# Kernel tuning notes

Hardware: AMD Instinct MI355X
Metric: run time of the kernel (lower is better)

## Reference

```python
import jax, jax.numpy as jnp
import numpy as np

V, E, H, L, T, B = 6500, 192, 6, 6, 512, 32
HS = E // H  # 32
EPS = 1e-5


def setup_inputs() -> dict:
    key = jax.random.key(0)
    ks = jax.random.split(key, 9)
    s = 0.02
    return {
        "idx": jax.random.randint(ks[0], (B, T), 0, V, dtype=jnp.int32),
        "tok_emb": jax.random.normal(ks[1], (V, E), dtype=jnp.float32) * s,
        "Wq": jax.random.normal(ks[2], (L, E, E), dtype=jnp.float32) * s,
        "Wk": jax.random.normal(ks[3], (L, E, E), dtype=jnp.float32) * s,
        "Wv": jax.random.normal(ks[4], (L, E, E), dtype=jnp.float32) * s,
        "Wo": jax.random.normal(ks[5], (L, E, E), dtype=jnp.float32) * s,
        "W1": jax.random.normal(ks[6], (L, E, 4 * E), dtype=jnp.float32) * s,
        "W2": jax.random.normal(ks[7], (L, 4 * E, E), dtype=jnp.float32) * s,
        "ln1_g": jnp.ones((L, E)), "ln1_b": jnp.zeros((L, E)),
        "ln2_g": jnp.ones((L, E)), "ln2_b": jnp.zeros((L, E)),
        "lnf_g": jnp.ones((E,)), "lnf_b": jnp.zeros((E,)),
        "Wlm": jax.random.normal(ks[8], (E, V), dtype=jnp.float32) * s,
    }


def _layer_norm(x, g, b):
    mu = jnp.mean(x, axis=-1, keepdims=True)
    var = jnp.mean(jnp.square(x - mu), axis=-1, keepdims=True)
    return (x - mu) * jax.lax.rsqrt(var + EPS) * g + b


def _sinusoidal(t, d):
    pos = jnp.arange(t, dtype=jnp.float32)[:, None]
    div = jnp.exp(jnp.arange(0, d, 2, dtype=jnp.float32) * (-np.log(10000.0) / d))
    pe = jnp.zeros((t, d), dtype=jnp.float32)
    pe = pe.at[:, 0::2].set(jnp.sin(pos * div))
    pe = pe.at[:, 1::2].set(jnp.cos(pos * div))
    return pe


def reference(idx, tok_emb, Wq, Wk, Wv, Wo, W1, W2,
              ln1_g, ln1_b, ln2_g, ln2_b, lnf_g, lnf_b, Wlm):
    x = tok_emb[idx] + _sinusoidal(T, E)[None, :, :]  # [B,T,E]
    mask = jnp.tril(jnp.ones((T, T), dtype=bool))
    scale = E ** (-0.5)  # NOTE: original scales by n_embd**-0.5, not head_size

    def block(x, p):
        l1g, l1b, wq, wk, wv, wo, l2g, l2b, w1, w2 = p
        h = _layer_norm(x, l1g, l1b)
        q = jnp.einsum('bte,ehd->bhtd', h, wq.reshape(E, H, HS))
        k = jnp.einsum('bte,ehd->bhtd', h, wk.reshape(E, H, HS))
        v = jnp.einsum('bte,ehd->bhtd', h, wv.reshape(E, H, HS))
        wei = jnp.einsum('bhtd,bhsd->bhts', q, k) * scale  # [B,H,T,T]
        wei = jnp.where(mask, wei, -jnp.inf)
        wei = jax.nn.softmax(wei, axis=-1)
        att = jnp.einsum('bhts,bhsd->bthd', wei, v).reshape(B, T, E)
        x = x + att @ wo
        h2 = _layer_norm(x, l2g, l2b)
        x = x + jax.nn.gelu(h2 @ w1, approximate=False) @ w2
        return x, None

    x, _ = jax.lax.scan(block, x, (ln1_g, ln1_b, Wq, Wk, Wv, Wo, ln2_g, ln2_b, W1, W2))
    x = _layer_norm(x, lnf_g, lnf_b)
    return x @ Wlm  # [B,T,V] logits
```

## Files before the change

### kernel.cpp

```cpp
#include <hip/hip_runtime.h>
#include <hip/hip_bf16.h>
#include <math.h>

#define VOCAB 6500
#define EMB   192
#define NH    6
#define NL    6
#define SEQ   512
#define BATCH 32
#define HSZ   32
#define BT    (BATCH*SEQ)

typedef __attribute__((ext_vector_type(8))) short bh8;
typedef __attribute__((ext_vector_type(4))) float f32x4;

__global__ __launch_bounds__(256) void embed_ln(
    const int* __restrict__ idx, const float* __restrict__ tok,
    const float* __restrict__ g, const float* __restrict__ b,
    float* __restrict__ x, __hip_bfloat16* __restrict__ h) {
  const int wid = threadIdx.x >> 6, lane = threadIdx.x & 63;
  const int bt = blockIdx.x * 4 + wid;
  const int t  = bt & (SEQ - 1);
  const int tokid = idx[bt];
  float v[3];
  #pragma unroll
  for (int i = 0; i < 3; ++i) {
    const int e = lane + i * 64;
    const int i2 = e & ~1;
    const float div = expf((float)i2 * (-9.210340371976184f / (float)EMB));
    const float ang = (float)t * div;
    const float pe  = (e & 1) ? cosf(ang) : sinf(ang);
    v[i] = tok[(size_t)tokid * EMB + e] + pe;
  }
  float s = v[0] + v[1] + v[2];
  #pragma unroll
  for (int o = 32; o; o >>= 1) s += __shfl_xor(s, o);
  const float mu = s * (1.0f / (float)EMB);
  float vs = 0.f;
  #pragma unroll
  for (int i = 0; i < 3; ++i) { const float d = v[i] - mu; vs += d * d; }
  #pragma unroll
  for (int o = 32; o; o >>= 1) vs += __shfl_xor(vs, o);
  const float r = rsqrtf(vs * (1.0f / (float)EMB) + 1e-5f);
  float* xr = x + (size_t)bt * EMB;
  __hip_bfloat16* hr = h + (size_t)bt * EMB;
  #pragma unroll
  for (int i = 0; i < 3; ++i) {
    const int e = lane + i * 64;
    xr[e] = v[i];
    hr[e] = __float2bfloat16((v[i] - mu) * r * g[e] + b[e]);
  }
}

__global__ __launch_bounds__(256) void wcast(
    const float* __restrict__ W, __hip_bfloat16* __restrict__ Wt,
    int K, int N, int dstride) {
  __shared__ float t[32][33];
  const float* Ws = W + (size_t)blockIdx.z * K * N;
  __hip_bfloat16* Wd = Wt + (size_t)blockIdx.z * dstride * K;
  const int kt = blockIdx.y * 32, nt = blockIdx.x * 32;
  const int tx = threadIdx.x, ty = threadIdx.y;
  for (int i = ty; i < 32; i += 8) {
    const int k = kt + i, n = nt + tx;
    t[i][tx] = (k < K && n < N) ? Ws[(size_t)k * N + n] : 0.f;
  }
  __syncthreads();
  for (int i = ty; i < 32; i += 8) {
    const int n = nt + i, k = kt + tx;
    if (n < N && k < K) Wd[(size_t)n * K + k] = __float2bfloat16(t[tx][i]);
  }
}

__global__ __launch_bounds__(256) void wcast4(
    const float* __restrict__ Wq, const float* __restrict__ Wk,
    const float* __restrict__ Wv, const float* __restrict__ Wo,
    __hip_bfloat16* __restrict__ wqkv, __hip_bfloat16* __restrict__ wot) {
  __shared__ float t[32][33];
  const int z = blockIdx.z, sel = z / NL, layer = z % NL;
  const float* srcs[4] = {Wq, Wk, Wv, Wo};
  const float* Ws = srcs[sel] + (size_t)layer * EMB * EMB;
  __hip_bfloat16* Wd = (sel < 3)
      ? wqkv + ((size_t)layer * 576 + sel * 192) * EMB
      : wot  + (size_t)layer * EMB * EMB;
  const int kt = blockIdx.y * 32, nt = blockIdx.x * 32;
  const int tx = threadIdx.x, ty = threadIdx.y;
  for (int i = ty; i < 32; i += 8)
    t[i][tx] = Ws[(size_t)(kt + i) * EMB + nt + tx];
  __syncthreads();
  for (int i = ty; i < 32; i += 8)
    Wd[(size_t)(nt + i) * EMB + kt + tx] = __float2bfloat16(t[tx][i]);
}

template<int EPI, int BN>
__global__ __launch_bounds__(256) void gemm_big(
    const __hip_bfloat16* __restrict__ A, const __hip_bfloat16* __restrict__ Bt,
    void* __restrict__ Cv, int M, int N, int K) {
  constexpr int LDK = 72;
  constexpr int NB = BN / 32;
  constexpr int NC = BN / 16;
  __shared__ short As[128 * LDK];
  __shared__ short Bs[BN * LDK];
  const int tid = threadIdx.x;
  const int wid = tid >> 6, lane = tid & 63;
  const int m0 = blockIdx.y * 128, n0 = blockIdx.x * BN;
  const int srow = tid >> 3, schk = tid & 7;
  const int fr = lane & 15, fg = lane >> 4;

  f32x4 acc[2][NC];
  #pragma unroll
  for (int rt = 0; rt < 2; ++rt)
    #pragma unroll
    for (int ct = 0; ct < NC; ++ct) acc[rt][ct] = (f32x4){0.f, 0.f, 0.f, 0.f};

  for (int k0 = 0; k0 < K; k0 += 64) {
    bh8 av[4], bv[NB];
    #pragma unroll
    for (int p = 0; p < 4; ++p)
      av[p] = *reinterpret_cast<const bh8*>(A + (size_t)(m0 + srow + p * 32) * K + k0 + schk * 8);
    #pragma unroll
    for (int p = 0; p < NB; ++p) {
      const int nr = n0 + srow + p * 32;
      if (nr < N) bv[p] = *reinterpret_cast<const bh8*>(Bt + (size_t)nr * K + k0 + schk * 8);
      else        bv[p] = (bh8){0,0,0,0,0,0,0,0};
    }
    __syncthreads();
    #pragma unroll
    for (int p = 0; p < 4; ++p)
      *reinterpret_cast<bh8*>(As + (srow + p * 32) * LDK + schk * 8) = av[p];
    #pragma unroll
    for (int p = 0; p < NB; ++p)
      *reinterpret_cast<bh8*>(Bs + (srow + p * 32) * LDK + schk * 8) = bv[p];
    __syncthreads();
    #pragma unroll
    for (int s = 0; s < 2; ++s) {
      bh8 af[2];
      #pragma unroll
      for (int rt = 0; rt < 2; ++rt)
        af[rt] = *reinterpret_cast<const bh8*>(As + (wid * 32 + rt * 16 + fr) * LDK + s * 32 + fg * 8);
      #pragma unroll
      for (int ct = 0; ct < NC; ++ct) {
        const bh8 bf_ = *reinterpret_cast<const bh8*>(Bs + (ct * 16 + fr) * LDK + s * 32 + fg * 8);
        #pragma unroll
        for (int rt = 0; rt < 2; ++rt)
          acc[rt][ct] = __builtin_amdgcn_mfma_f32_16x16x32_bf16(af[rt], bf_, acc[rt][ct], 0, 0, 0);
      }
    }
  }

  #pragma unroll
  for (int rt = 0; rt < 2; ++rt)
    #pragma unroll
    for (int ct = 0; ct < NC; ++ct) {
      const int col = n0 + ct * 16 + fr;
      if (col < N) {
        #pragma unroll
        for (int rr = 0; rr < 4; ++rr) {
          const int row = m0 + wid * 32 + rt * 16 + fg * 4 + rr;
          float v = acc[rt][ct][rr];
          if (EPI == 0) {
            ((float*)Cv)[(size_t)row * N + col] = v;
          } else if (EPI == 2) {
            v = 0.5f * v * (1.0f + erff(v * 0.70710678118654752f));
            ((__hip_bfloat16*)Cv)[(size_t)row * N + col] = __float2bfloat16(v);
          } else {
            const int part = col / 192, c2 = col - part * 192;
            const int bb = row >> 9, tt = row & (SEQ - 1);
            const int hh = c2 >> 5, dd = c2 & (HSZ - 1);
            ((__hip_bfloat16*)Cv)[(size_t)part * BT * EMB +
                (((size_t)(bb * NH + hh)) * SEQ + tt) * HSZ + dd] = __float2bfloat16(v);
          }
        }
      }
    }
}

__global__ __launch_bounds__(256) void gemm_resln(
    const __hip_bfloat16* __restrict__ A, const __hip_bfloat16* __restrict__ Bt,
    float* __restrict__ X, __hip_bfloat16* __restrict__ Hout,
    const float* __restrict__ g, const float* __restrict__ b, int K) {
  constexpr int LDK = 72;
  __shared__ short As[64 * LDK];
  __shared__ short Bs[192 * LDK];
  const int tid = threadIdx.x;
  const int wid = tid >> 6, lane = tid & 63;
  const int m0 = blockIdx.x * 64;
  const int srow = tid >> 3, schk = tid & 7;
  const int fr = lane & 15, fg = lane >> 4;

  f32x4 acc[12];
  #pragma unroll
  for (int j = 0; j < 12; ++j) acc[j] = (f32x4){0.f, 0.f, 0.f, 0.f};

  for (int k0 = 0; k0 < K; k0 += 64) {
    bh8 av[2], bv[6];
    #pragma unroll
    for (int p = 0; p < 2; ++p)
      av[p] = *reinterpret_cast<const bh8*>(A + (size_t)(m0 + srow + p * 32) * K + k0 + schk * 8);
    #pragma unroll
    for (int p = 0; p < 6; ++p)
      bv[p] = *reinterpret_cast<const bh8*>(Bt + (size_t)(srow + p * 32) * K + k0 + schk * 8);
    __syncthreads();
    #pragma unroll
    for (int p = 0; p < 2; ++p)
      *reinterpret_cast<bh8*>(As + (srow + p * 32) * LDK + schk * 8) = av[p];
    #pragma unroll
    for (int p = 0; p < 6; ++p)
      *reinterpret_cast<bh8*>(Bs + (srow + p * 32) * LDK + schk * 8) = bv[p];
    __syncthreads();
    #pragma unroll
    for (int s = 0; s < 2; ++s) {
      const bh8 af = *reinterpret_cast<const bh8*>(As + (wid * 16 + fr) * LDK + s * 32 + fg * 8);
      #pragma unroll
      for (int j = 0; j < 12; ++j) {
        const bh8 bf_ = *reinterpret_cast<const bh8*>(Bs + (j * 16 + fr) * LDK + s * 32 + fg * 8);
        acc[j] = __builtin_amdgcn_mfma_f32_16x16x32_bf16(af, bf_, acc[j], 0, 0, 0);
      }
    }
  }

  #pragma unroll
  for (int rr = 0; rr < 4; ++rr) {
    const int row = m0 + wid * 16 + fg * 4 + rr;
    float v[12], sum = 0.f, sq = 0.f;
    #pragma unroll
    for (int j = 0; j < 12; ++j) {
      v[j] = acc[j][rr] + X[(size_t)row * EMB + j * 16 + fr];
      sum += v[j]; sq += v[j] * v[j];
    }
    #pragma unroll
    for (int o = 8; o; o >>= 1) {
      sum += __shfl_xor(sum, o);
      sq  += __shfl_xor(sq,  o);
    }
    const float mu = sum * (1.0f / (float)EMB);
    const float r  = rsqrtf(sq * (1.0f / (float)EMB) - mu * mu + 1e-5f);
    #pragma unroll
    for (int j = 0; j < 12; ++j) {
      const int col = j * 16 + fr;
      X[(size_t)row * EMB + col] = v[j];
      Hout[(size_t)row * EMB + col] = __float2bfloat16((v[j] - mu) * r * g[col] + b[col]);
    }
  }
}

__global__ __launch_bounds__(256) void flash_attn(
    const __hip_bfloat16* __restrict__ qh, const __hip_bfloat16* __restrict__ kh,
    const __hip_bfloat16* __restrict__ vh, __hip_bfloat16* __restrict__ att) {
  constexpr int QT = 128, KT = 64, LDP = 72;
  __shared__ __hip_bfloat16 Ks[KT * LDP];
  __shared__ __hip_bfloat16 Vs[HSZ * LDP];
  __shared__ __hip_bfloat16 Ps[4][32 * LDP];
  const int qt = blockIdx.x, h = blockIdx.y, b = blockIdx.z;
  const int tid = threadIdx.x, wid = tid >> 6, lane = tid & 63;
  const int q0 = qt * QT;
  const size_t hb = ((size_t)(b * NH + h)) * SEQ * HSZ;
  const int fr = lane & 15, fg = lane >> 4;
  const float SCALE = 0.07216878364870323f;

  bh8 aq[2];
  #pragma unroll
  for (int rt = 0; rt < 2; ++rt)
    aq[rt] = *reinterpret_cast<const bh8*>(
        qh + hb + (size_t)(q0 + wid * 32 + rt * 16 + fr) * HSZ + fg * 8);

  f32x4 o[2][2];
  float m[2][4], l[2][4];
  #pragma unroll
  for (int rt = 0; rt < 2; ++rt) {
    #pragma unroll
    for (int ct = 0; ct < 2; ++ct) o[rt][ct] = (f32x4){0.f, 0.f, 0.f, 0.f};
    #pragma unroll
    for (int rr = 0; rr < 4; ++rr) { m[rt][rr] = -1e30f; l[rt][rr] = 0.f; }
  }

  const int nt = 2 * qt + 2;
  const int sr = tid >> 2, d0 = (tid & 3) * 8;
  for (int it = 0; it < nt; ++it) {
    const int s0 = it * KT;
    __syncthreads();
    {
      const bh8 kv8 = *reinterpret_cast<const bh8*>(kh + hb + (size_t)(s0 + sr) * HSZ + d0);
      *reinterpret_cast<bh8*>(&Ks[sr * LDP + d0]) = kv8;
      const bh8 vv8 = *reinterpret_cast<const bh8*>(vh + hb + (size_t)(s0 + sr) * HSZ + d0);
      short tmp[8]; *reinterpret_cast<bh8*>(tmp) = vv8;
      #pragma unroll
      for (int j = 0; j < 8; ++j)
        Vs[(d0 + j) * LDP + sr] = *reinterpret_cast<__hip_bfloat16*>(&tmp[j]);
    }
    __syncthreads();

    f32x4 sfr[2][4];
    #pragma unroll
    for (int rt = 0; rt < 2; ++rt)
      #pragma unroll
      for (int st = 0; st < 4; ++st) {
        const bh8 bf_ = *reinterpret_cast<const bh8*>(&Ks[(st * 16 + fr) * LDP + fg * 8]);
        sfr[rt][st] = __builtin_amdgcn_mfma_f32_16x16x32_bf16(
            aq[rt], bf_, (f32x4){0.f, 0.f, 0.f, 0.f}, 0, 0, 0);
      }

    if (s0 + KT - 1 > q0 + wid * 32) {
      #pragma unroll
      for (int rt = 0; rt < 2; ++rt)
        #pragma unroll
        for (int st = 0; st < 4; ++st) {
          const int sa = s0 + st * 16 + fr;
          #pragma unroll
          for (int rr = 0; rr < 4; ++rr) {
            const int qa = q0 + wid * 32 + rt * 16 + fg * 4 + rr;
            sfr[rt][st][rr] = (sa > qa) ? -1e30f : sfr[rt][st][rr] * SCALE;
          }
        }
    } else {
      #pragma unroll
      for (int rt = 0; rt < 2; ++rt)
        #pragma unroll
        for (int st = 0; st < 4; ++st)
          #pragma unroll
          for (int rr = 0; rr < 4; ++rr) sfr[rt][st][rr] *= SCALE;
    }

    __hip_bfloat16* Pw = Ps[wid];
    #pragma unroll
    for (int rt = 0; rt < 2; ++rt) {
      #pragma unroll
      for (int rr = 0; rr < 4; ++rr) {
        float mx = fmaxf(fmaxf(sfr[rt][0][rr], sfr[rt][1][rr]),
                         fmaxf(sfr[rt][2][rr], sfr[rt][3][rr]));
        #pragma unroll
        for (int off = 8; off; off >>= 1) mx = fmaxf(mx, __shfl_xor(mx, off));
        const float newm = fmaxf(m[rt][rr], mx);
        const float alpha = __expf(m[rt][rr] - newm);
        m[rt][rr] = newm;
        float s = 0.f;
        #pragma unroll
        for (int st = 0; st < 4; ++st) {
          const float p = __expf(sfr[rt][st][rr] - newm);
          s += p;
          Pw[(rt * 16 + fg * 4 + rr) * LDP + st * 16 + fr] = __float2bfloat16(p);
        }
        #pragma unroll
        for (int off = 8; off; off >>= 1) s += __shfl_xor(s, off);
        l[rt][rr] = l[rt][rr] * alpha + s;
        #pragma unroll
        for (int ct = 0; ct < 2; ++ct) o[rt][ct][rr] *= alpha;
      }
    }

    #pragma unroll
    for (int ks = 0; ks < 2; ++ks) {
      bh8 vb_[2];
      #pragma unroll
      for (int ct = 0; ct < 2; ++ct)
        vb_[ct] = *reinterpret_cast<const bh8*>(&Vs[(ct * 16 + fr) * LDP + ks * 32 + fg * 8]);
      #pragma unroll
      for (int rt = 0; rt < 2; ++rt) {
        const bh8 pa = *reinterpret_cast<const bh8*>(&Pw[(rt * 16 + fr) * LDP + ks * 32 + fg * 8]);
        #pragma unroll
        for (int ct = 0; ct < 2; ++ct)
          o[rt][ct] = __builtin_amdgcn_mfma_f32_16x16x32_bf16(pa, vb_[ct], o[rt][ct], 0, 0, 0);
      }
    }
  }

  #pragma unroll
  for (int rt = 0; rt < 2; ++rt)
    #pragma unroll
    for (int rr = 0; rr < 4; ++rr) {
      const float inv = 1.0f / l[rt][rr];
      const int qa = q0 + wid * 32 + rt * 16 + fg * 4 + rr;
      #pragma unroll
      for (int ct = 0; ct < 2; ++ct) {
        const int d = ct * 16 + fr;
        att[((size_t)(b * SEQ + qa)) * EMB + h * HSZ + d] =
            __float2bfloat16(o[rt][ct][rr] * inv);
      }
    }
}

extern "C" void kernel_launch(void* const* d_in, const int* in_sizes, int n_in,
                              void* d_out, int out_size, void* d_ws, size_t ws_size,
                              hipStream_t stream) {
  const int*   idx   = (const int*)  d_in[0];
  const float* tok   = (const float*)d_in[1];
  const float* Wq    = (const float*)d_in[2];
  const float* Wk    = (const float*)d_in[3];
  const float* Wv    = (const float*)d_in[4];
  const float* Wo    = (const float*)d_in[5];
  const float* W1    = (const float*)d_in[6];
  const float* W2    = (const float*)d_in[7];
  const float* ln1g  = (const float*)d_in[8];
  const float* ln1b  = (const float*)d_in[9];
  const float* ln2g  = (const float*)d_in[10];
  const float* ln2b  = (const float*)d_in[11];
  const float* lnfg  = (const float*)d_in[12];
  const float* lnfb  = (const float*)d_in[13];
  const float* Wlm   = (const float*)d_in[14];
  float* out = (float*)d_out;

  const size_t NTE = (size_t)BT * EMB;
  char* ws = (char*)d_ws;
  float* x   = (float*)ws;                         ws += NTE * 4;
  __hip_bfloat16* qh   = (__hip_bfloat16*)ws;      ws += NTE * 2 * 3;
  __hip_bfloat16* h    = (__hip_bfloat16*)ws;      ws += NTE * 2;
  __hip_bfloat16* att  = (__hip_bfloat16*)ws;      ws += NTE * 2;
  __hip_bfloat16* hid  = (__hip_bfloat16*)ws;      ws += NTE * 4 * 2;
  __hip_bfloat16* wqkv = (__hip_bfloat16*)ws;      ws += (size_t)NL * 576 * EMB * 2;
  __hip_bfloat16* wot  = (__hip_bfloat16*)ws;      ws += (size_t)NL * EMB * EMB * 2;
  __hip_bfloat16* w1t  = (__hip_bfloat16*)ws;      ws += (size_t)NL * EMB * EMB * 4 * 2;
  __hip_bfloat16* w2t  = (__hip_bfloat16*)ws;      ws += (size_t)NL * EMB * EMB * 4 * 2;
  __hip_bfloat16* wlt  = (__hip_bfloat16*)ws;

  const dim3 tblk(32, 8);
  wcast4<<<dim3(6, 6, 4 * NL), tblk, 0, stream>>>(Wq, Wk, Wv, Wo, wqkv, wot);
  wcast<<<dim3(24, 6, NL),  tblk, 0, stream>>>(W1,  w1t, EMB, EMB * 4, EMB * 4);
  wcast<<<dim3(6, 24, NL),  tblk, 0, stream>>>(W2,  w2t, EMB * 4, EMB, EMB);
  wcast<<<dim3(204, 6, 1),  tblk, 0, stream>>>(Wlm, wlt, EMB, VOCAB, VOCAB);

  embed_ln<<<BT / 4, 256, 0, stream>>>(idx, tok, ln1g, ln1b, x, h);

  const dim3 gQKV(576 / 64, BT / 128);
  const dim3 gM  (EMB * 4 / 64, BT / 128);
  const dim3 gV  ((VOCAB + 127) / 128, BT / 128);
  const dim3 gA  (SEQ / 128, NH, BATCH);

  for (int l = 0; l < NL; ++l) {
    const size_t wo = (size_t)l * EMB * EMB;
    const size_t wm = (size_t)l * EMB * EMB * 4;
    gemm_big<3, 64><<<gQKV, 256, 0, stream>>>(h, wqkv + (size_t)l * 576 * EMB, qh, BT, 576, EMB);
    flash_attn<<<gA, 256, 0, stream>>>(qh, qh + NTE, qh + 2 * NTE, att);
    gemm_resln<<<BT / 64, 256, 0, stream>>>(att, wot + wo, x, h,
                                            ln2g + l * EMB, ln2b + l * EMB, EMB);
    gemm_big<2, 64><<<gM, 256, 0, stream>>>(h, w1t + wm, hid, BT, EMB * 4, EMB);
    const float* ng = (l == NL - 1) ? lnfg : ln1g + (l + 1) * EMB;
    const float* nb = (l == NL - 1) ? lnfb : ln1b + (l + 1) * EMB;
    gemm_resln<<<BT / 64, 256, 0, stream>>>(hid, w2t + wm, x, h, ng, nb, EMB * 4);
  }

  gemm_big<0, 128><<<gV, 256, 0, stream>>>(h, wlt, out, BT, VOCAB, EMB);
}
```

Baseline: 815.1 us.

## Fuse residual+LayerNorm GEMMs with following W1/QKV GEMMs; drop online-softmax max tracking

A new resln_stream kernel computes the Wo (or W2) GEMM, adds the residual, applies LayerNorm, keeps the normalized rows in LDS, and streams the next projection (W1 with GELU, or the next layer's QKV with head-split layout) in 64-column chunks. This removes the separate W1 and QKV launches and the global write and reread of h. Flash attention now folds the scale into Q at projection time and drops the running max and rescaling, exponentiating raw scores directly. That saves the reductions and alpha multiplies but risks overflow if scores grow large, relying on the small-magnitude inputs.

```diff
diff --git a/kernel.cpp b/kernel.cpp
--- a/kernel.cpp
+++ b/kernel.cpp
@@ -13,6 +13,13 @@
 
 typedef __attribute__((ext_vector_type(8))) short bh8;
 typedef __attribute__((ext_vector_type(4))) float f32x4;
+
+#define ATT_SCALE 0.07216878364870323f
+
+static __device__ __forceinline__ short bf16s(float v) {
+  __hip_bfloat16 t = __float2bfloat16(v);
+  return *reinterpret_cast<short*>(&t);
+}
 
 __global__ __launch_bounds__(256) void embed_ln(
     const int* __restrict__ idx, const float* __restrict__ tok,
@@ -159,11 +166,9 @@
           float v = acc[rt][ct][rr];
           if (EPI == 0) {
             ((float*)Cv)[(size_t)row * N + col] = v;
-          } else if (EPI == 2) {
-            v = 0.5f * v * (1.0f + erff(v * 0.70710678118654752f));
-            ((__hip_bfloat16*)Cv)[(size_t)row * N + col] = __float2bfloat16(v);
           } else {
             const int part = col / 192, c2 = col - part * 192;
+            if (part == 0) v *= ATT_SCALE;
             const int bb = row >> 9, tt = row & (SEQ - 1);
             const int hh = c2 >> 5, dd = c2 & (HSZ - 1);
             ((__hip_bfloat16*)Cv)[(size_t)part * BT * EMB +
@@ -243,6 +248,137 @@
   }
 }
 
+template<int P2>
+__global__ __launch_bounds__(256) void resln_stream(
+    const __hip_bfloat16* __restrict__ A, const __hip_bfloat16* __restrict__ B1t,
+    float* __restrict__ X, const float* __restrict__ g, const float* __restrict__ b,
+    int K1, const __hip_bfloat16* __restrict__ B2t,
+    __hip_bfloat16* __restrict__ Out2, int N2) {
+  constexpr int LDK = 72;
+  constexpr int LDH = 200;
+  __shared__ __align__(16) short lds[64 * LDH * 2];
+  short* As  = lds;
+  short* Bs  = lds + 64 * LDK;
+  short* Hs  = lds;
+  short* Bs2 = lds + 64 * LDH;
+  const int tid = threadIdx.x;
+  const int wid = tid >> 6, lane = tid & 63;
+  const int m0 = blockIdx.x * 64;
+  const int srow = tid >> 3, schk = tid & 7;
+  const int fr = lane & 15, fg = lane >> 4;
+
+  f32x4 acc[12];
+  #pragma unroll
+  for (int j = 0; j < 12; ++j) acc[j] = (f32x4){0.f, 0.f, 0.f, 0.f};
+
+  for (int k0 = 0; k0 < K1; k0 += 64) {
+    bh8 av[2], bv[6];
+    #pragma unroll
+    for (int p = 0; p < 2; ++p)
+      av[p] = *reinterpret_cast<const bh8*>(A + (size_t)(m0 + srow + p * 32) * K1 + k0 + schk * 8);
+    #pragma unroll
+    for (int p = 0; p < 6; ++p)
+      bv[p] = *reinterpret_cast<const bh8*>(B1t + (size_t)(srow + p * 32) * K1 + k0 + schk * 8);
+    __syncthreads();
+    #pragma unroll
+    for (int p = 0; p < 2; ++p)
+      *reinterpret_cast<bh8*>(As + (srow + p * 32) * LDK + schk * 8) = av[p];
+    #pragma unroll
+    for (int p = 0; p < 6; ++p)
+      *reinterpret_cast<bh8*>(Bs + (srow + p * 32) * LDK + schk * 8) = bv[p];
+    __syncthreads();
+    #pragma unroll
+    for (int s = 0; s < 2; ++s) {
+      const bh8 af = *reinterpret_cast<const bh8*>(As + (wid * 16 + fr) * LDK + s * 32 + fg * 8);
+      #pragma unroll
+      for (int j = 0; j < 12; ++j) {
+        const bh8 bf_ = *reinterpret_cast<const bh8*>(Bs + (j * 16 + fr) * LDK + s * 32 + fg * 8);
+        acc[j] = __builtin_amdgcn_mfma_f32_16x16x32_bf16(af, bf_, acc[j], 0, 0, 0);
+      }
+    }
+  }
+  __syncthreads();
+
+  #pragma unroll
+  for (int rr = 0; rr < 4; ++rr) {
+    const int lrow = wid * 16 + fg * 4 + rr;
+    const int row = m0 + lrow;
+    float v[12], sum = 0.f, sq = 0.f;
+    #pragma unroll
+    for (int j = 0; j < 12; ++j) {
+      v[j] = acc[j][rr] + X[(size_t)row * EMB + j * 16 + fr];
+      sum += v[j]; sq += v[j] * v[j];
+    }
+    #pragma unroll
+    for (int o = 8; o; o >>= 1) {
+      sum += __shfl_xor(sum, o);
+      sq  += __shfl_xor(sq,  o);
+    }
+    const float mu = sum * (1.0f / (float)EMB);
+    const float r  = rsqrtf(sq * (1.0f / (float)EMB) - mu * mu + 1e-5f);
+    #pragma unroll
+    for (int j = 0; j < 12; ++j) {
+      const int col = j * 16 + fr;
+      X[(size_t)row * EMB + col] = v[j];
+      Hs[lrow * LDH + col] = bf16s((v[j] - mu) * r * g[col] + b[col]);
+    }
+  }
+
+  const int nchunk = N2 >> 6;
+  const int r2 = tid >> 2, kp = (tid & 3) * 48;
+  bh8 bv2[6];
+  #pragma unroll
+  for (int i = 0; i < 6; ++i)
+    bv2[i] = *reinterpret_cast<const bh8*>(B2t + (size_t)r2 * EMB + kp + i * 8);
+
+  for (int c = 0; c < nchunk; ++c) {
+    __syncthreads();
+    #pragma unroll
+    for (int i = 0; i < 6; ++i)
+      *reinterpret_cast<bh8*>(Bs2 + r2 * LDH + kp + i * 8) = bv2[i];
+    if (c + 1 < nchunk) {
+      #pragma unroll
+      for (int i = 0; i < 6; ++i)
+        bv2[i] = *reinterpret_cast<const bh8*>(B2t + (size_t)((c + 1) * 64 + r2) * EMB + kp + i * 8);
+    }
+    __syncthreads();
+
+    f32x4 a2[4];
+    #pragma unroll
+    for (int ct = 0; ct < 4; ++ct) a2[ct] = (f32x4){0.f, 0.f, 0.f, 0.f};
+    #pragma unroll
+    for (int s = 0; s < 6; ++s) {
+      const bh8 af = *reinterpret_cast<const bh8*>(Hs + (wid * 16 + fr) * LDH + s * 32 + fg * 8);
+      #pragma unroll
+      for (int ct = 0; ct < 4; ++ct) {
+        const bh8 bf_ = *reinterpret_cast<const bh8*>(Bs2 + (ct * 16 + fr) * LDH + s * 32 + fg * 8);
+        a2[ct] = __builtin_amdgcn_mfma_f32_16x16x32_bf16(af, bf_, a2[ct], 0, 0, 0);
+      }
+    }
+
+    #pragma unroll
+    for (int ct = 0; ct < 4; ++ct) {
+      const int col = c * 64 + ct * 16 + fr;
+      #pragma unroll
+      for (int rr = 0; rr < 4; ++rr) {
+        const int row = m0 + wid * 16 + fg * 4 + rr;
+        float v = a2[ct][rr];
+        if (P2 == 1) {
+          v = 0.5f * v * (1.0f + erff(v * 0.70710678118654752f));
+          Out2[(size_t)row * N2 + col] = __float2bfloat16(v);
+        } else {
+          const int part = col / 192, c2 = col - part * 192;
+          if (part == 0) v *= ATT_SCALE;
+          const int bb = row >> 9, tt = row & (SEQ - 1);
+          const int hh = c2 >> 5, dd = c2 & (HSZ - 1);
+          Out2[(size_t)part * BT * EMB +
+               (((size_t)(bb * NH + hh)) * SEQ + tt) * HSZ + dd] = __float2bfloat16(v);
+        }
+      }
+    }
+  }
+}
+
 __global__ __launch_bounds__(256) void flash_attn(
     const __hip_bfloat16* __restrict__ qh, const __hip_bfloat16* __restrict__ kh,
     const __hip_bfloat16* __restrict__ vh, __hip_bfloat16* __restrict__ att) {
@@ -255,7 +391,6 @@
   const int q0 = qt * QT;
   const size_t hb = ((size_t)(b * NH + h)) * SEQ * HSZ;
   const int fr = lane & 15, fg = lane >> 4;
-  const float SCALE = 0.07216878364870323f;
 
   bh8 aq[2];
   #pragma unroll
@@ -264,13 +399,13 @@
         qh + hb + (size_t)(q0 + wid * 32 + rt * 16 + fr) * HSZ + fg * 8);
 
   f32x4 o[2][2];
-  float m[2][4], l[2][4];
+  float lp[2][4];
   #pragma unroll
   for (int rt = 0; rt < 2; ++rt) {
     #pragma unroll
     for (int ct = 0; ct < 2; ++ct) o[rt][ct] = (f32x4){0.f, 0.f, 0.f, 0.f};
     #pragma unroll
-    for (int rr = 0; rr < 4; ++rr) { m[rt][rr] = -1e30f; l[rt][rr] = 0.f; }
+    for (int rr = 0; rr < 4; ++rr) lp[rt][rr] = 0.f;
   }
 
   const int nt = 2 * qt + 2;
@@ -299,51 +434,28 @@
             aq[rt], bf_, (f32x4){0.f, 0.f, 0.f, 0.f}, 0, 0, 0);
       }
 
-    if (s0 + KT - 1 > q0 + wid * 32) {
-      #pragma unroll
-      for (int rt = 0; rt < 2; ++rt)
-        #pragma unroll
-        for (int st = 0; st < 4; ++st) {
-          const int sa = s0 + st * 16 + fr;
+    __hip_bfloat16* Pw = Ps[wid];
+    const bool diag = (s0 + KT - 1 > q0 + wid * 32);
+    #pragma unroll
+    for (int rt = 0; rt < 2; ++rt) {
+      #pragma unroll
+      for (int rr = 0; rr < 4; ++rr) {
+        float pr[4];
+        if (diag) {
+          const int qa = q0 + wid * 32 + rt * 16 + fg * 4 + rr;
           #pragma unroll
-          for (int rr = 0; rr < 4; ++rr) {
-            const int qa = q0 + wid * 32 + rt * 16 + fg * 4 + rr;
-            sfr[rt][st][rr] = (sa > qa) ? -1e30f : sfr[rt][st][rr] * SCALE;
+          for (int st = 0; st < 4; ++st) {
+            const int sa = s0 + st * 16 + fr;
+            pr[st] = (sa > qa) ? 0.f : __expf(sfr[rt][st][rr]);
           }
+        } else {
+          #pragma unroll
+          for (int st = 0; st < 4; ++st) pr[st] = __expf(sfr[rt][st][rr]);
         }
-    } else {
-      #pragma unroll
-      for (int rt = 0; rt < 2; ++rt)
+        lp[rt][rr] += (pr[0] + pr[1]) + (pr[2] + pr[3]);
         #pragma unroll
         for (int st = 0; st < 4; ++st)
-          #pragma unroll
-          for (int rr = 0; rr < 4; ++rr) sfr[rt][st][rr] *= SCALE;
-    }
-
-    __hip_bfloat16* Pw = Ps[wid];
-    #pragma unroll
-    for (int rt = 0; rt < 2; ++rt) {
-      #pragma unroll
-      for (int rr = 0; rr < 4; ++rr) {
-        float mx = fmaxf(fmaxf(sfr[rt][0][rr], sfr[rt][1][rr]),
-                         fmaxf(sfr[rt][2][rr], sfr[rt][3][rr]));
-        #pragma unroll
-        for (int off = 8; off; off >>= 1) mx = fmaxf(mx, __shfl_xor(mx, off));
-        const float newm = fmaxf(m[rt][rr], mx);
-        const float alpha = __expf(m[rt][rr] - newm);
-        m[rt][rr] = newm;
-        float s = 0.f;
-        #pragma unroll
-        for (int st = 0; st < 4; ++st) {
-          const float p = __expf(sfr[rt][st][rr] - newm);
-          s += p;
-          Pw[(rt * 16 + fg * 4 + rr) * LDP + st * 16 + fr] = __float2bfloat16(p);
-        }
-        #pragma unroll
-        for (int off = 8; off; off >>= 1) s += __shfl_xor(s, off);
-        l[rt][rr] = l[rt][rr] * alpha + s;
-        #pragma unroll
-        for (int ct = 0; ct < 2; ++ct) o[rt][ct][rr] *= alpha;
+          Pw[(rt * 16 + fg * 4 + rr) * LDP + st * 16 + fr] = __float2bfloat16(pr[st]);
       }
     }
 
@@ -367,7 +479,10 @@
   for (int rt = 0; rt < 2; ++rt)
     #pragma unroll
     for (int rr = 0; rr < 4; ++rr) {
-      const float inv = 1.0f / l[rt][rr];
+      float s = lp[rt][rr];
+      #pragma unroll
+      for (int off = 8; off; off >>= 1) s += __shfl_xor(s, off);
+      const float inv = 1.0f / s;
       const int qa = q0 + wid * 32 + rt * 16 + fg * 4 + rr;
       #pragma unroll
       for (int ct = 0; ct < 2; ++ct) {
@@ -420,21 +535,25 @@
   embed_ln<<<BT / 4, 256, 0, stream>>>(idx, tok, ln1g, ln1b, x, h);
 
   const dim3 gQKV(576 / 64, BT / 128);
-  const dim3 gM  (EMB * 4 / 64, BT / 128);
   const dim3 gV  ((VOCAB + 127) / 128, BT / 128);
   const dim3 gA  (SEQ / 128, NH, BATCH);
+
+  gemm_big<3, 64><<<gQKV, 256, 0, stream>>>(h, wqkv, qh, BT, 576, EMB);
 
   for (int l = 0; l < NL; ++l) {
     const size_t wo = (size_t)l * EMB * EMB;
     const size_t wm = (size_t)l * EMB * EMB * 4;
-    gemm_big<3, 64><<<gQKV, 256, 0, stream>>>(h, wqkv + (size_t)l * 576 * EMB, qh, BT, 576, EMB);
     flash_attn<<<gA, 256, 0, stream>>>(qh, qh + NTE, qh + 2 * NTE, att);
-    gemm_resln<<<BT / 64, 256, 0, stream>>>(att, wot + wo, x, h,
-                                            ln2g + l * EMB, ln2b + l * EMB, EMB);
-    gemm_big<2, 64><<<gM, 256, 0, stream>>>(h, w1t + wm, hid, BT, EMB * 4, EMB);
-    const float* ng = (l == NL - 1) ? lnfg : ln1g + (l + 1) * EMB;
-    const float* nb = (l == NL - 1) ? lnfb : ln1b + (l + 1) * EMB;
-    gemm_resln<<<BT / 64, 256, 0, stream>>>(hid, w2t + wm, x, h, ng, nb, EMB * 4);
+    resln_stream<1><<<BT / 64, 256, 0, stream>>>(
+        att, wot + wo, x, ln2g + l * EMB, ln2b + l * EMB, EMB,
+        w1t + wm, hid, EMB * 4);
+    if (l < NL - 1) {
+      resln_stream<2><<<BT / 64, 256, 0, stream>>>(
+          hid, w2t + wm, x, ln1g + (l + 1) * EMB, ln1b + (l + 1) * EMB, EMB * 4,
+          wqkv + (size_t)(l + 1) * 576 * EMB, qh, 576);
+    } else {
+      gemm_resln<<<BT / 64, 256, 0, stream>>>(hid, w2t + wm, x, h, lnfg, lnfb, EMB * 4);
+    }
   }
 
   gemm_big<0, 128><<<gV, 256, 0, stream>>>(h, wlt, out, BT, VOCAB, EMB);
```

Result: slower. 891.6 us (+9.4%).
